# Performance work log

Hardware: AMD Instinct MI355X
Metric: run time of the kernel (lower is better)

Reference implementation:

```python
import jax, jax.numpy as jnp
import numpy as np

B, T, C, E, K = 4, 4096, 2048, 64, 8


def setup_inputs() -> dict:
    key = jax.random.key(0)
    k1, k2, k3 = jax.random.split(key, 3)
    hidden_states = jax.random.normal(k1, (B, T, C), dtype=jnp.float32)
    mask = jax.random.randint(k2, (B, T), 0, 2).astype(bool)
    gate_weight = jax.random.normal(k3, (E, C), dtype=jnp.float32) * 0.02
    gate_bias = jnp.zeros((E,), dtype=jnp.float32)
    expert_biases = jnp.zeros((E,), dtype=jnp.float32)
    return {
        "hidden_states": hidden_states,
        "mask": mask,
        "gate_weight": gate_weight,
        "gate_bias": gate_bias,
        "expert_biases": expert_biases,
    }


def reference(hidden_states, mask, gate_weight, gate_bias, expert_biases):
    Bc, Tc, Cc = hidden_states.shape
    n_experts = gate_weight.shape[0]
    x = hidden_states.reshape(-1, Cc)                 # [N, C]
    m = mask.reshape(-1)                              # [N]
    gate_output = x @ gate_weight.T + gate_bias       # [N, E]
    gate_probs = jax.nn.sigmoid(gate_output)
    gate_logits = gate_output + expert_biases
    _, top_k_indices = jax.lax.top_k(gate_logits, K)  # [N, K]
    top_k_probs = jnp.take_along_axis(gate_probs, top_k_indices, axis=-1)
    top_k_probs = top_k_probs / jnp.sum(top_k_probs, axis=-1, keepdims=True)
    # masked bincount of routed experts (only tokens where mask is True)
    weights = jnp.broadcast_to(m[:, None], top_k_indices.shape).astype(jnp.float32)
    expert_counts = jnp.zeros((n_experts,), jnp.float32).at[top_k_indices.reshape(-1)].add(weights.reshape(-1))
    avg_count = expert_counts.mean()
    maxvio = (expert_counts.max() - avg_count) / (avg_count + 1e-5)
    # note: the in-place expert_biases sign-update is a training-time, no-grad
    # side effect and does not change the returned values of this call.
    return top_k_indices, top_k_probs, maxvio
```

## Files before the change

### kernel.cpp

```cpp
#include <hip/hip_runtime.h>
#include <math.h>

#define NTOK   16384
#define CDIM   2048
#define NEXP   64
#define TOPK   8
#define KSPLIT 4
#define RBLK   1024

typedef _Float16 f16x8 __attribute__((ext_vector_type(8)));
typedef float    f32x4 __attribute__((ext_vector_type(4)));

__global__ __launch_bounds__(256) void pack_w16_kernel(
    const float* __restrict__ W,
    _Float16* __restrict__ Wh, _Float16* __restrict__ Wl)
{
    int t    = blockIdx.x * 256 + threadIdx.x;
    int lane = t & 63;
    int nt   = (t >> 6) & 3;
    int s    = t >> 8;
    int e    = nt * 16 + (lane & 15);
    int k    = s * 32 + (lane >> 4) * 8;
    const float* src = W + (size_t)e * CDIM + k;
    #pragma unroll
    for (int j = 0; j < 8; j++) {
        float x = src[j];
        _Float16 h = (_Float16)x;
        Wh[(size_t)t * 8 + j] = h;
        Wl[(size_t)t * 8 + j] = (_Float16)(x - (float)h);
    }
}

__global__ __launch_bounds__(256, 4) void gemm_f16split_kernel(
    const float* __restrict__ x,
    const _Float16* __restrict__ Wh,
    const _Float16* __restrict__ Wl,
    float* __restrict__ part)
{
    const int lane = threadIdx.x & 63;
    const int wid  = threadIdx.x >> 6;
    const int tb   = blockIdx.x & 255;
    const int pp   = blockIdx.x >> 8;
    const int tok0 = tb * 64 + wid * 16;
    const int q    = lane >> 4;
    const size_t xbase = (size_t)(tok0 + (lane & 15)) * CDIM + pp * 512 + q * 8;

    f32x4 acc[4];
    #pragma unroll
    for (int nt = 0; nt < 4; nt++) acc[nt] = (f32x4){0.f, 0.f, 0.f, 0.f};

    for (int s = 0; s < 16; s++) {
        const int S = pp * 16 + s;
        float4 v0 = *(const float4*)&x[xbase + s * 32];
        float4 v1 = *(const float4*)&x[xbase + s * 32 + 4];
        float xr[8] = {v0.x, v0.y, v0.z, v0.w, v1.x, v1.y, v1.z, v1.w};
        f16x8 ah, al;
        #pragma unroll
        for (int j = 0; j < 8; j++) {
            _Float16 h = (_Float16)xr[j];
            ah[j] = h;
            al[j] = (_Float16)(xr[j] - (float)h);
        }
        const f16x8* bhp = (const f16x8*)(Wh + ((size_t)S * 4 * 64 + lane) * 8);
        const f16x8* blp = (const f16x8*)(Wl + ((size_t)S * 4 * 64 + lane) * 8);
        #pragma unroll
        for (int nt = 0; nt < 4; nt++) {
            f16x8 bh = bhp[nt * 64];
            f16x8 bl = blp[nt * 64];
            acc[nt] = __builtin_amdgcn_mfma_f32_16x16x32_f16(ah, bh, acc[nt], 0, 0, 0);
            acc[nt] = __builtin_amdgcn_mfma_f32_16x16x32_f16(al, bh, acc[nt], 0, 0, 0);
            acc[nt] = __builtin_amdgcn_mfma_f32_16x16x32_f16(ah, bl, acc[nt], 0, 0, 0);
        }
    }

    #pragma unroll
    for (int nt = 0; nt < 4; nt++) {
        #pragma unroll
        for (int r = 0; r < 4; r++) {
            size_t tok = (size_t)tok0 + q * 4 + r;
            part[((size_t)pp * NTOK + tok) * NEXP + nt * 16 + (lane & 15)] = acc[nt][r];
        }
    }
}

__global__ __launch_bounds__(256) void reduce_topk_kernel(
    const float* __restrict__ part,
    const int*   __restrict__ mask,
    const float* __restrict__ gbias,
    const float* __restrict__ ebias,
    float*       __restrict__ out,
    float*       __restrict__ blockcnt)
{
    __shared__ unsigned int cnt[NEXP];
    const int tid = threadIdx.x;
    if (tid < NEXP) cnt[tid] = 0u;
    __syncthreads();

    const int t = blockIdx.x * 16 + (tid >> 4);
    const int l = tid & 15;

    float4 v = make_float4(0.f, 0.f, 0.f, 0.f);
    #pragma unroll
    for (int p = 0; p < KSPLIT; p++) {
        float4 u = *(const float4*)&part[((size_t)p * NTOK + t) * NEXP + l * 4];
        v.x += u.x; v.y += u.y; v.z += u.z; v.w += u.w;
    }
    float4 gb = *(const float4*)&gbias[l * 4];
    float4 eb = *(const float4*)&ebias[l * 4];
    float z[4], sel[4];
    z[0] = v.x + gb.x; z[1] = v.y + gb.y; z[2] = v.z + gb.z; z[3] = v.w + gb.w;
    sel[0] = z[0] + eb.x; sel[1] = z[1] + eb.y;
    sel[2] = z[2] + eb.z; sel[3] = z[3] + eb.w;

    int   idxs[TOPK];
    float probs[TOPK];
    float psum = 0.f;

    #pragma unroll
    for (int r = 0; r < TOPK; r++) {
        float bv = -INFINITY, bz = 0.f; int bidx = 1 << 30;
        #pragma unroll
        for (int i = 0; i < 4; i++)
            if (sel[i] > bv) { bv = sel[i]; bz = z[i]; bidx = l * 4 + i; }
        #pragma unroll
        for (int m = 1; m < 16; m <<= 1) {
            float ov = __shfl_xor(bv, m);
            float oz = __shfl_xor(bz, m);
            int   oi = __shfl_xor(bidx, m);
            if (ov > bv || (ov == bv && oi < bidx)) { bv = ov; bz = oz; bidx = oi; }
        }
        idxs[r] = bidx;
        float p = 1.f / (1.f + expf(-bz));
        probs[r] = p; psum += p;
        if ((bidx >> 2) == l) sel[bidx & 3] = -INFINITY;
    }

    float inv = 1.f / psum;
    if (l < TOPK) {
        out[(size_t)t * TOPK + l] = (float)idxs[l];
        out[(size_t)NTOK * TOPK + (size_t)t * TOPK + l] = probs[l] * inv;
        if (mask[t] != 0) atomicAdd(&cnt[idxs[l]], 1u);
    }
    __syncthreads();
    if (tid < NEXP)
        blockcnt[(size_t)blockIdx.x * NEXP + tid] = (float)cnt[tid];
}

__global__ __launch_bounds__(256) void finalize_kernel(
    const float* __restrict__ blockcnt, float* __restrict__ out)
{
    __shared__ float ps[4][NEXP];
    const int t = threadIdx.x;
    const int e = t & 63, c = t >> 6;
    float s = 0.f;
    #pragma unroll 8
    for (int b = 0; b < RBLK / 4; b++)
        s += blockcnt[(size_t)(c * (RBLK / 4) + b) * NEXP + e];
    ps[c][e] = s;
    __syncthreads();
    if (t < 64) {
        float tot = ps[0][t] + ps[1][t] + ps[2][t] + ps[3][t];
        float mx = tot, sm = tot;
        #pragma unroll
        for (int o = 32; o > 0; o >>= 1) {
            mx = fmaxf(mx, __shfl_down(mx, o));
            sm += __shfl_down(sm, o);
        }
        if (t == 0) {
            float avg = sm / (float)NEXP;
            out[2 * NTOK * TOPK] = (mx - avg) / (avg + 1e-5f);
        }
    }
}

__global__ __launch_bounds__(256) void fused_fallback_kernel(
    const float* __restrict__ x, const int* __restrict__ mask,
    const float* __restrict__ W, const float* __restrict__ gbias,
    const float* __restrict__ ebias, float* __restrict__ out,
    unsigned int* __restrict__ counts)
{
    __shared__ float As[64][36];
    __shared__ float Bs[64][36];
    __shared__ float Lg[64][NEXP + 1];
    __shared__ float s_gb[NEXP], s_eb[NEXP];
    __shared__ unsigned int s_cnt[NEXP];
    const int tid = threadIdx.x;
    const int tx = tid & 15, ty = tid >> 4;
    const int m0 = blockIdx.x * 64;
    if (tid < NEXP) { s_gb[tid] = gbias[tid]; s_eb[tid] = ebias[tid]; s_cnt[tid] = 0u; }
    float acc[4][4] = {};
    for (int kb = 0; kb < CDIM; kb += 32) {
        __syncthreads();
        #pragma unroll
        for (int p = 0; p < 2; p++) {
            int lin = tid + p * 256; int m = lin >> 3; int c4 = (lin & 7) << 2;
            *(float4*)&As[m][c4] = *(const float4*)&x[(size_t)(m0 + m) * CDIM + kb + c4];
            *(float4*)&Bs[m][c4] = *(const float4*)&W[(size_t)m * CDIM + kb + c4];
        }
        __syncthreads();
        #pragma unroll
        for (int k4 = 0; k4 < 32; k4 += 4) {
            float4 a[4], b[4];
            #pragma unroll
            for (int i = 0; i < 4; i++) a[i] = *(const float4*)&As[ty * 4 + i][k4];
            #pragma unroll
            for (int j = 0; j < 4; j++) b[j] = *(const float4*)&Bs[tx * 4 + j][k4];
            #pragma unroll
            for (int i = 0; i < 4; i++)
                #pragma unroll
                for (int j = 0; j < 4; j++)
                    acc[i][j] += a[i].x * b[j].x + a[i].y * b[j].y
                               + a[i].z * b[j].z + a[i].w * b[j].w;
        }
    }
    __syncthreads();
    #pragma unroll
    for (int i = 0; i < 4; i++)
        #pragma unroll
        for (int j = 0; j < 4; j++)
            Lg[ty * 4 + i][tx * 4 + j] = acc[i][j] + s_gb[tx * 4 + j];
    __syncthreads();
    if (tid < 64) {
        const int g = m0 + tid;
        unsigned long long used = 0ull;
        int idxs[TOPK]; float probs[TOPK]; float psum = 0.f;
        #pragma unroll
        for (int k = 0; k < TOPK; k++) {
            float best = -INFINITY; int bi = 0;
            for (int n = 0; n < NEXP; n++) {
                if ((used >> n) & 1ull) continue;
                float vv = Lg[tid][n] + s_eb[n];
                if (vv > best) { best = vv; bi = n; }
            }
            used |= (1ull << bi);
            idxs[k] = bi;
            float p = 1.f / (1.f + expf(-Lg[tid][bi]));
            probs[k] = p; psum += p;
        }
        float inv = 1.f / psum;
        #pragma unroll
        for (int k = 0; k < TOPK; k++) {
            out[(size_t)g * TOPK + k] = (float)idxs[k];
            out[(size_t)NTOK * TOPK + (size_t)g * TOPK + k] = probs[k] * inv;
        }
        if (mask[g] != 0)
            #pragma unroll
            for (int k = 0; k < TOPK; k++) atomicAdd(&s_cnt[idxs[k]], 1u);
    }
    __syncthreads();
    if (tid < NEXP && s_cnt[tid] != 0u) atomicAdd(&counts[tid], s_cnt[tid]);
}

__global__ void finalize_atomic_kernel(const unsigned int* __restrict__ counts,
                                       float* __restrict__ out)
{
    const int t = threadIdx.x;
    float c  = (float)counts[t];
    float mx = c, sm = c;
    #pragma unroll
    for (int o = 32; o > 0; o >>= 1) {
        mx = fmaxf(mx, __shfl_down(mx, o));
        sm += __shfl_down(sm, o);
    }
    if (t == 0) {
        float avg = sm / (float)NEXP;
        out[2 * NTOK * TOPK] = (mx - avg) / (avg + 1e-5f);
    }
}

extern "C" void kernel_launch(void* const* d_in, const int* in_sizes, int n_in,
                              void* d_out, int out_size, void* d_ws, size_t ws_size,
                              hipStream_t stream)
{
    const float* x     = (const float*)d_in[0];
    const int*   mask  = (const int*)  d_in[1];
    const float* W     = (const float*)d_in[2];
    const float* gbias = (const float*)d_in[3];
    const float* ebias = (const float*)d_in[4];
    float* out = (float*)d_out;

    const size_t whB  = (size_t)NEXP * CDIM * sizeof(_Float16);
    const size_t bcB  = (size_t)RBLK * NEXP * sizeof(float);
    const size_t ptB  = (size_t)KSPLIT * NTOK * NEXP * sizeof(float);
    const size_t need = 2 * whB + bcB + ptB;

    if (ws_size >= need) {
        _Float16* Wh = (_Float16*)d_ws;
        _Float16* Wl = (_Float16*)((char*)d_ws + whB);
        float* blockcnt = (float*)((char*)d_ws + 2 * whB);
        float* part = (float*)((char*)d_ws + 2 * whB + bcB);

        pack_w16_kernel<<<64, 256, 0, stream>>>(W, Wh, Wl);
        gemm_f16split_kernel<<<256 * KSPLIT, 256, 0, stream>>>(x, Wh, Wl, part);
        reduce_topk_kernel<<<RBLK, 256, 0, stream>>>(part, mask, gbias, ebias, out, blockcnt);
        finalize_kernel<<<1, 256, 0, stream>>>(blockcnt, out);
        return;
    }

    unsigned int* counts = (unsigned int*)d_ws;
    hipMemsetAsync(d_ws, 0, NEXP * sizeof(unsigned int), stream);
    fused_fallback_kernel<<<NTOK / 64, 256, 0, stream>>>(x, mask, W, gbias, ebias, out, counts);
    finalize_atomic_kernel<<<1, 64, 0, stream>>>(counts, out);
}
```

Before: 233.2 us.

## Fuse gate GEMM with top-k routing and drop split-K partials

Merges the split-K MFMA GEMM and the reduce/top-k kernel into one kernel that accumulates the full 2048-wide dot product per wave and then does top-k, sigmoid normalization and masked expert counting from registers. This removes the partial-sum buffer write/read and one kernel launch. It adds register double-buffering of x and weight fragments across K steps. The grid shrinks to 256 blocks, which lowers wave-level parallelism for hiding the memory latency of streaming x.

```diff
diff --git a/kernel.cpp b/kernel.cpp
--- a/kernel.cpp
+++ b/kernel.cpp
@@ -5,8 +5,7 @@
 #define CDIM   2048
 #define NEXP   64
 #define TOPK   8
-#define KSPLIT 4
-#define RBLK   1024
+#define GBLK   256
 
 typedef _Float16 f16x8 __attribute__((ext_vector_type(8)));
 typedef float    f32x4 __attribute__((ext_vector_type(4)));
@@ -31,60 +30,31 @@
     }
 }
 
-__global__ __launch_bounds__(256, 4) void gemm_f16split_kernel(
+__device__ __forceinline__ void mfma_step(
+    const float4 v0, const float4 v1,
+    const f16x8* __restrict__ bh, const f16x8* __restrict__ bl,
+    f32x4* __restrict__ acc)
+{
+    float xr[8] = {v0.x, v0.y, v0.z, v0.w, v1.x, v1.y, v1.z, v1.w};
+    f16x8 ah, al;
+    #pragma unroll
+    for (int j = 0; j < 8; j++) {
+        _Float16 h = (_Float16)xr[j];
+        ah[j] = h;
+        al[j] = (_Float16)(xr[j] - (float)h);
+    }
+    #pragma unroll
+    for (int nt = 0; nt < 4; nt++) {
+        acc[nt] = __builtin_amdgcn_mfma_f32_16x16x32_f16(ah, bh[nt], acc[nt], 0, 0, 0);
+        acc[nt] = __builtin_amdgcn_mfma_f32_16x16x32_f16(al, bh[nt], acc[nt], 0, 0, 0);
+        acc[nt] = __builtin_amdgcn_mfma_f32_16x16x32_f16(ah, bl[nt], acc[nt], 0, 0, 0);
+    }
+}
+
+__global__ __launch_bounds__(256, 4) void gate_fused_kernel(
     const float* __restrict__ x,
     const _Float16* __restrict__ Wh,
     const _Float16* __restrict__ Wl,
-    float* __restrict__ part)
-{
-    const int lane = threadIdx.x & 63;
-    const int wid  = threadIdx.x >> 6;
-    const int tb   = blockIdx.x & 255;
-    const int pp   = blockIdx.x >> 8;
-    const int tok0 = tb * 64 + wid * 16;
-    const int q    = lane >> 4;
-    const size_t xbase = (size_t)(tok0 + (lane & 15)) * CDIM + pp * 512 + q * 8;
-
-    f32x4 acc[4];
-    #pragma unroll
-    for (int nt = 0; nt < 4; nt++) acc[nt] = (f32x4){0.f, 0.f, 0.f, 0.f};
-
-    for (int s = 0; s < 16; s++) {
-        const int S = pp * 16 + s;
-        float4 v0 = *(const float4*)&x[xbase + s * 32];
-        float4 v1 = *(const float4*)&x[xbase + s * 32 + 4];
-        float xr[8] = {v0.x, v0.y, v0.z, v0.w, v1.x, v1.y, v1.z, v1.w};
-        f16x8 ah, al;
-        #pragma unroll
-        for (int j = 0; j < 8; j++) {
-            _Float16 h = (_Float16)xr[j];
-            ah[j] = h;
-            al[j] = (_Float16)(xr[j] - (float)h);
-        }
-        const f16x8* bhp = (const f16x8*)(Wh + ((size_t)S * 4 * 64 + lane) * 8);
-        const f16x8* blp = (const f16x8*)(Wl + ((size_t)S * 4 * 64 + lane) * 8);
-        #pragma unroll
-        for (int nt = 0; nt < 4; nt++) {
-            f16x8 bh = bhp[nt * 64];
-            f16x8 bl = blp[nt * 64];
-            acc[nt] = __builtin_amdgcn_mfma_f32_16x16x32_f16(ah, bh, acc[nt], 0, 0, 0);
-            acc[nt] = __builtin_amdgcn_mfma_f32_16x16x32_f16(al, bh, acc[nt], 0, 0, 0);
-            acc[nt] = __builtin_amdgcn_mfma_f32_16x16x32_f16(ah, bl, acc[nt], 0, 0, 0);
-        }
-    }
-
-    #pragma unroll
-    for (int nt = 0; nt < 4; nt++) {
-        #pragma unroll
-        for (int r = 0; r < 4; r++) {
-            size_t tok = (size_t)tok0 + q * 4 + r;
-            part[((size_t)pp * NTOK + tok) * NEXP + nt * 16 + (lane & 15)] = acc[nt][r];
-        }
-    }
-}
-
-__global__ __launch_bounds__(256) void reduce_topk_kernel(
-    const float* __restrict__ part,
     const int*   __restrict__ mask,
     const float* __restrict__ gbias,
     const float* __restrict__ ebias,
@@ -92,54 +62,94 @@
     float*       __restrict__ blockcnt)
 {
     __shared__ unsigned int cnt[NEXP];
-    const int tid = threadIdx.x;
+    const int tid  = threadIdx.x;
+    const int lane = tid & 63;
+    const int wid  = tid >> 6;
     if (tid < NEXP) cnt[tid] = 0u;
     __syncthreads();
 
-    const int t = blockIdx.x * 16 + (tid >> 4);
-    const int l = tid & 15;
-
-    float4 v = make_float4(0.f, 0.f, 0.f, 0.f);
-    #pragma unroll
-    for (int p = 0; p < KSPLIT; p++) {
-        float4 u = *(const float4*)&part[((size_t)p * NTOK + t) * NEXP + l * 4];
-        v.x += u.x; v.y += u.y; v.z += u.z; v.w += u.w;
-    }
-    float4 gb = *(const float4*)&gbias[l * 4];
-    float4 eb = *(const float4*)&ebias[l * 4];
-    float z[4], sel[4];
-    z[0] = v.x + gb.x; z[1] = v.y + gb.y; z[2] = v.z + gb.z; z[3] = v.w + gb.w;
-    sel[0] = z[0] + eb.x; sel[1] = z[1] + eb.y;
-    sel[2] = z[2] + eb.z; sel[3] = z[3] + eb.w;
-
-    int   idxs[TOPK];
-    float probs[TOPK];
-    float psum = 0.f;
-
-    #pragma unroll
-    for (int r = 0; r < TOPK; r++) {
-        float bv = -INFINITY, bz = 0.f; int bidx = 1 << 30;
-        #pragma unroll
-        for (int i = 0; i < 4; i++)
-            if (sel[i] > bv) { bv = sel[i]; bz = z[i]; bidx = l * 4 + i; }
-        #pragma unroll
-        for (int m = 1; m < 16; m <<= 1) {
-            float ov = __shfl_xor(bv, m);
-            float oz = __shfl_xor(bz, m);
-            int   oi = __shfl_xor(bidx, m);
-            if (ov > bv || (ov == bv && oi < bidx)) { bv = ov; bz = oz; bidx = oi; }
-        }
-        idxs[r] = bidx;
-        float p = 1.f / (1.f + expf(-bz));
-        probs[r] = p; psum += p;
-        if ((bidx >> 2) == l) sel[bidx & 3] = -INFINITY;
-    }
-
-    float inv = 1.f / psum;
-    if (l < TOPK) {
-        out[(size_t)t * TOPK + l] = (float)idxs[l];
-        out[(size_t)NTOK * TOPK + (size_t)t * TOPK + l] = probs[l] * inv;
-        if (mask[t] != 0) atomicAdd(&cnt[idxs[l]], 1u);
+    const int tok0 = blockIdx.x * 64 + wid * 16;
+    const int col  = lane & 15;
+    const int q    = lane >> 4;
+    const float* xp = x + (size_t)(tok0 + col) * CDIM + q * 8;
+    const f16x8* bhp = (const f16x8*)Wh + lane;
+    const f16x8* blp = (const f16x8*)Wl + lane;
+
+    f32x4 acc[4];
+    #pragma unroll
+    for (int nt = 0; nt < 4; nt++) acc[nt] = (f32x4){0.f, 0.f, 0.f, 0.f};
+
+    float4 a0v0, a0v1, a1v0, a1v1;
+    f16x8 b0h[4], b0l[4], b1h[4], b1l[4];
+
+    a0v0 = *(const float4*)(xp);
+    a0v1 = *(const float4*)(xp + 4);
+    #pragma unroll
+    for (int nt = 0; nt < 4; nt++) { b0h[nt] = bhp[nt * 64]; b0l[nt] = blp[nt * 64]; }
+
+    for (int s = 0; s < 64; s += 2) {
+        a1v0 = *(const float4*)(xp + (s + 1) * 32);
+        a1v1 = *(const float4*)(xp + (s + 1) * 32 + 4);
+        #pragma unroll
+        for (int nt = 0; nt < 4; nt++) {
+            b1h[nt] = bhp[(s + 1) * 256 + nt * 64];
+            b1l[nt] = blp[(s + 1) * 256 + nt * 64];
+        }
+        mfma_step(a0v0, a0v1, b0h, b0l, acc);
+
+        const int s2 = (s + 2 < 64) ? (s + 2) : 63;
+        a0v0 = *(const float4*)(xp + s2 * 32);
+        a0v1 = *(const float4*)(xp + s2 * 32 + 4);
+        #pragma unroll
+        for (int nt = 0; nt < 4; nt++) {
+            b0h[nt] = bhp[s2 * 256 + nt * 64];
+            b0l[nt] = blp[s2 * 256 + nt * 64];
+        }
+        mfma_step(a1v0, a1v1, b1h, b1l, acc);
+    }
+
+    float gb[4], eb[4];
+    #pragma unroll
+    for (int nt = 0; nt < 4; nt++) {
+        gb[nt] = gbias[nt * 16 + col];
+        eb[nt] = ebias[nt * 16 + col];
+    }
+
+    #pragma unroll
+    for (int r = 0; r < 4; r++) {
+        const int t = tok0 + q * 4 + r;
+        float z[4], sel[4];
+        #pragma unroll
+        for (int nt = 0; nt < 4; nt++) {
+            z[nt]   = acc[nt][r] + gb[nt];
+            sel[nt] = z[nt] + eb[nt];
+        }
+
+        int idxs[TOPK]; float probs[TOPK]; float psum = 0.f;
+        #pragma unroll
+        for (int rr = 0; rr < TOPK; rr++) {
+            float bv = -INFINITY, bz = 0.f; int bidx = 1 << 30;
+            #pragma unroll
+            for (int nt = 0; nt < 4; nt++)
+                if (sel[nt] > bv) { bv = sel[nt]; bz = z[nt]; bidx = nt * 16 + col; }
+            #pragma unroll
+            for (int m = 1; m < 16; m <<= 1) {
+                float ov = __shfl_xor(bv, m);
+                float oz = __shfl_xor(bz, m);
+                int   oi = __shfl_xor(bidx, m);
+                if (ov > bv || (ov == bv && oi < bidx)) { bv = ov; bz = oz; bidx = oi; }
+            }
+            idxs[rr] = bidx;
+            float p = 1.f / (1.f + expf(-bz));
+            probs[rr] = p; psum += p;
+            if ((bidx & 15) == col) sel[bidx >> 4] = -INFINITY;
+        }
+        float inv = 1.f / psum;
+        if (col < TOPK) {
+            out[(size_t)t * TOPK + col] = (float)idxs[col];
+            out[(size_t)NTOK * TOPK + (size_t)t * TOPK + col] = probs[col] * inv;
+            if (mask[t] != 0) atomicAdd(&cnt[idxs[col]], 1u);
+        }
     }
     __syncthreads();
     if (tid < NEXP)
@@ -154,8 +164,8 @@
     const int e = t & 63, c = t >> 6;
     float s = 0.f;
     #pragma unroll 8
-    for (int b = 0; b < RBLK / 4; b++)
-        s += blockcnt[(size_t)(c * (RBLK / 4) + b) * NEXP + e];
+    for (int b = 0; b < GBLK / 4; b++)
+        s += blockcnt[(size_t)(c * (GBLK / 4) + b) * NEXP + e];
     ps[c][e] = s;
     __syncthreads();
     if (t < 64) {
@@ -280,19 +290,16 @@
     float* out = (float*)d_out;
 
     const size_t whB  = (size_t)NEXP * CDIM * sizeof(_Float16);
-    const size_t bcB  = (size_t)RBLK * NEXP * sizeof(float);
-    const size_t ptB  = (size_t)KSPLIT * NTOK * NEXP * sizeof(float);
-    const size_t need = 2 * whB + bcB + ptB;
+    const size_t bcB  = (size_t)GBLK * NEXP * sizeof(float);
+    const size_t need = 2 * whB + bcB;
 
     if (ws_size >= need) {
         _Float16* Wh = (_Float16*)d_ws;
         _Float16* Wl = (_Float16*)((char*)d_ws + whB);
         float* blockcnt = (float*)((char*)d_ws + 2 * whB);
-        float* part = (float*)((char*)d_ws + 2 * whB + bcB);
 
         pack_w16_kernel<<<64, 256, 0, stream>>>(W, Wh, Wl);
-        gemm_f16split_kernel<<<256 * KSPLIT, 256, 0, stream>>>(x, Wh, Wl, part);
-        reduce_topk_kernel<<<RBLK, 256, 0, stream>>>(part, mask, gbias, ebias, out, blockcnt);
+        gate_fused_kernel<<<GBLK, 256, 0, stream>>>(x, Wh, Wl, mask, gbias, ebias, out, blockcnt);
         finalize_kernel<<<1, 256, 0, stream>>>(blockcnt, out);
         return;
     }
```

Measured after the change: 270.1 us. +15.8%, slower.
